# Kernel optimization log

Hardware: AMD Instinct MI355X
Metric: run time of the kernel (lower is better)

Reference implementation:

```python
import jax, jax.numpy as jnp
import numpy as np

H = 256        # hidden_channels (== out_channels)
IN = 128       # in_channels (atom features)
ED = 64        # edge_dim (bond features)
G = 1024       # num graphs
L = 48         # atoms per graph (static pad length)
N = G * L      # num atoms
E = 2 * N      # num directed edges
NLAYERS = 4


def setup_inputs() -> dict:
    key = jax.random.key(0)
    ks = jax.random.split(key, 12)
    def rn(k, shape, scale=0.05):
        return jax.random.normal(k, shape, jnp.float32) * scale
    return {
        "x": jax.random.normal(ks[0], (N, IN), jnp.float32),
        "edge_attr": jax.random.normal(ks[1], (E, ED), jnp.float32),
        "edge_index": jax.random.randint(ks[2], (2, E), 0, N),
        "batch": jnp.repeat(jnp.arange(G), L),  # sorted, L atoms per graph
        "w_atom": rn(ks[3], (IN, H)), "b_atom": jnp.zeros((H,), jnp.float32),
        "w_bond": rn(ks[4], (ED, H)), "b_bond": jnp.zeros((H,), jnp.float32),
        "conv_w": rn(ks[5], (NLAYERS, H, H)), "conv_b": jnp.zeros((NLAYERS, H), jnp.float32),
        "w_lin": rn(ks[6], (3 * H, H)), "b_lin": jnp.zeros((H,), jnp.float32),
        "gru_bias": rn(ks[7], (H,), 0.06),
        "w_ih": rn(ks[8], (2, 3 * H, H)), "w_hh": rn(ks[9], (2, 3 * H, H)),
        "b_ih": jnp.zeros((2, 3 * H), jnp.float32), "b_hh": jnp.zeros((2, 3 * H), jnp.float32),
        "w_out": rn(ks[10], (2 * H, H)), "b_out": jnp.zeros((H,), jnp.float32),
    }


def reference(x, edge_attr, edge_index, batch, w_atom, b_atom, w_bond, b_bond,
              conv_w, conv_b, w_lin, b_lin, gru_bias, w_ih, w_hh, b_ih, b_hh,
              w_out, b_out):
    relu = jax.nn.relu
    row, col = edge_index[0], edge_index[1]  # flow='target_to_source': aggregate at row

    x_proj = relu(x @ w_atom + b_atom)                 # [N, H]
    h_atom = x_proj
    h_bond = relu(edge_attr @ w_bond + b_bond)         # [E, H]

    def booster(h_bond):
        # message_booster multi-aggregation: sum * max (empty slots -> 0, as torch_scatter)
        s = jax.ops.segment_sum(h_bond, row, num_segments=N)
        m = jax.ops.segment_max(h_bond, row, num_segments=N)
        m = jnp.where(jnp.isfinite(m), m, 0.0)
        return s * m

    for i in range(NLAYERS - 1):
        h_atom = h_atom + booster(h_bond)              # additive communicator
        # edge_update: x[edge_index_i] - edge_attr[edge_index_j]; seq = Linear+ReLU (dropout p=0)
        h_bond = relu((h_atom[row] - h_bond[col]) @ conv_w[i] + conv_b[i])
    aggr_message = h_atom + booster(h_bond)            # last conv; edge output discarded

    h = jnp.concatenate([aggr_message, h_atom, x_proj], axis=1) @ w_lin + b_lin  # [N, H]

    # ---- BatchGRU ----
    msg = relu(h + gru_bias)
    starts = jnp.searchsorted(batch, jnp.arange(G))
    pos = jnp.arange(N) - starts[batch]                # position within own graph
    messages = jnp.zeros((G, L, H), h.dtype).at[batch, pos].set(msg)
    h0 = jax.ops.segment_max(h, batch, num_segments=G)  # [G, H], same init both dirs

    def gru_dir(seq, d):
        def cell(hst, x_t):
            gi = x_t @ w_ih[d].T + b_ih[d]
            gh = hst @ w_hh[d].T + b_hh[d]
            i_r, i_z, i_n = jnp.split(gi, 3, -1)
            h_r, h_z, h_n = jnp.split(gh, 3, -1)
            r = jax.nn.sigmoid(i_r + h_r)
            z = jax.nn.sigmoid(i_z + h_z)
            n = jnp.tanh(i_n + r * h_n)
            hn = (1.0 - z) * n + z * hst
            return hn, hn
        _, out = jax.lax.scan(cell, h0, seq)
        return out

    seq = messages.transpose(1, 0, 2)                  # [L, G, H]
    out_f = gru_dir(seq, 0)
    out_b = gru_dir(seq[::-1], 1)[::-1]
    h_msgs = jnp.concatenate([out_f, out_b], -1).transpose(1, 0, 2)  # [G, L, 2H]
    unpadded = h_msgs[batch, pos]                      # [N, 2H]

    return relu(unpadded @ w_out + b_out)              # seq_out (dropout p=0)
```

## Files before the change

### kernel.cpp

```cpp
#include <hip/hip_runtime.h>
#include <math.h>

#define HH 256
#define GG 1024
#define LL 48
#define NNODES 49152
#define NEDGES 98304
#define SB 256.0f
#define DSB 0.00390625f

typedef _Float16 f16;
typedef __attribute__((ext_vector_type(8))) _Float16 f16x8;
typedef __attribute__((ext_vector_type(4))) float f32x4;

#define MFMA16(a, b, c) __builtin_amdgcn_mfma_f32_16x16x32_f16(a, b, c, 0, 0, 0)

__device__ inline float sc_from_max(float m) {
    if (!(m > 0.f)) return 1.0f;
    return ldexpf(1.0f, 13 - ilogbf(m));
}

__global__ void csr_count(const int* __restrict__ row, int* __restrict__ counts)
{
    int e = blockIdx.x * 256 + threadIdx.x;
    if (e < NEDGES) atomicAdd(&counts[row[e]], 1);
}

__global__ __launch_bounds__(1024) void scan_offsets(const int* __restrict__ counts,
                                                     int* __restrict__ offsets)
{
    __shared__ int tsum[1024];
    const int tid = threadIdx.x;
    const int base = tid * 48;
    int s = 0;
    for (int i = 0; i < 48; i++) s += counts[base + i];
    tsum[tid] = s;
    __syncthreads();
    for (int off = 1; off < 1024; off <<= 1) {
        int v = (tid >= off) ? tsum[tid - off] : 0;
        __syncthreads();
        tsum[tid] += v;
        __syncthreads();
    }
    int run = (tid == 0) ? 0 : tsum[tid - 1];
    for (int i = 0; i < 48; i++) { offsets[base + i] = run; run += counts[base + i]; }
    if (tid == 1023) offsets[NNODES] = run;
}

__global__ void csr_fill(const int* __restrict__ row, const int* __restrict__ offsets,
                         int* __restrict__ cursor, int* __restrict__ elist)
{
    int e = blockIdx.x * 256 + threadIdx.x;
    if (e < NEDGES) {
        int r = row[e];
        int p = atomicAdd(&cursor[r], 1);
        elist[offsets[r] + p] = e;
    }
}

__global__ void prep_graphs(const int* __restrict__ batch, int* __restrict__ starts,
                            int* __restrict__ gcnt)
{
    int i = blockIdx.x * 256 + threadIdx.x;
    if (i < NNODES) {
        int b = batch[i];
        atomicAdd(&gcnt[b], 1);
        if (i == 0 || batch[i - 1] != b) starts[b] = i;
    }
}

__global__ void rowscale(const float* __restrict__ A, int K, float* __restrict__ sc)
{
    int m = blockIdx.x, ln = threadIdx.x;
    float v = 0.f;
    for (int k = ln; k < K; k += 64) v = fmaxf(v, fabsf(A[(size_t)m * K + k]));
    for (int s = 32; s; s >>= 1) v = fmaxf(v, __shfl_xor(v, s));
    if (ln == 0) sc[m] = sc_from_max(v);
}

__global__ void prep_wT(const float* __restrict__ Wsrc, f16* __restrict__ oH,
                        f16* __restrict__ oL)
{
    int idx = blockIdx.x * 256 + threadIdx.x;
    int k = idx >> 8, n = idx & 255;
    float v = Wsrc[(size_t)k * 256 + n] * SB;
    f16 h = (f16)v;
    size_t o = ((size_t)(k >> 5) * 256 + n) * 32 + (k & 31);
    oH[o] = h;
    oL[o] = (f16)(v - (float)h);
}

__global__ void prep_gruW(const float* __restrict__ w_ih, const float* __restrict__ w_hh,
                          const float* __restrict__ b_ih, const float* __restrict__ b_hh,
                          f16* __restrict__ BgH, f16* __restrict__ BgL,
                          float* __restrict__ bias4)
{
    int idx = blockIdx.x * 256 + threadIdx.x;
    int d = idx >> 19;
    int rem = idx & 524287;
    int k = rem >> 10;
    int col = rem & 1023;
    int jj = col >> 2, s = col & 3;
    const float* Wi = w_ih + (size_t)d * 768 * 256;
    const float* Wh = w_hh + (size_t)d * 768 * 256;
    float v;
    if (s == 0)      v = (k < 256) ? Wi[(size_t)jj * 256 + k]         : Wh[(size_t)jj * 256 + (k - 256)];
    else if (s == 1) v = (k < 256) ? Wi[(size_t)(256 + jj) * 256 + k] : Wh[(size_t)(256 + jj) * 256 + (k - 256)];
    else if (s == 2) v = (k < 256) ? Wi[(size_t)(512 + jj) * 256 + k] : 0.f;
    else             v = (k < 256) ? 0.f : Wh[(size_t)(512 + jj) * 256 + (k - 256)];
    v *= SB;
    f16 h = (f16)v;
    size_t o = ((size_t)(d * 16 + (k >> 5)) * 1024 + col) * 32 + (k & 31);
    BgH[o] = h;
    BgL[o] = (f16)(v - (float)h);
    if (k == 0) {
        const float* bi = b_ih + d * 768;
        const float* bh = b_hh + d * 768;
        float bv;
        if (s == 0)      bv = bi[jj] + bh[jj];
        else if (s == 1) bv = bi[256 + jj] + bh[256 + jj];
        else if (s == 2) bv = bi[512 + jj];
        else             bv = bh[512 + jj];
        bias4[d * 1024 + col] = bv;
    }
}

__global__ void booster(const float* __restrict__ hb_lo, const float* __restrict__ hb_hi,
                        const float* __restrict__ atom_in, float* __restrict__ out,
                        const int* __restrict__ offsets, const int* __restrict__ elist,
                        float* __restrict__ scOut)
{
    int n = blockIdx.x, c = threadIdx.x;
    int b0 = offsets[n], b1 = offsets[n + 1];
    float s = 0.f, m = 0.f;
    for (int p = b0; p < b1; p++) {
        int e = elist[p];
        const float* hb = (e < NNODES) ? (hb_lo + (size_t)e * HH)
                                       : (hb_hi + (size_t)(e - NNODES) * HH);
        float v = hb[c];
        s += v;
        m = fmaxf(m, v);
    }
    float o = atom_in[(size_t)n * HH + c] + s * m;
    out[(size_t)n * HH + c] = o;
    float v = fabsf(o);
    for (int t = 32; t; t >>= 1) v = fmaxf(v, __shfl_xor(v, t));
    __shared__ float wm[4];
    if ((c & 63) == 0) wm[c >> 6] = v;
    __syncthreads();
    if (c == 0)
        scOut[n] = sc_from_max(fmaxf(fmaxf(wm[0], wm[1]), fmaxf(wm[2], wm[3])));
}

__global__ void h0_init(const float* __restrict__ h, const int* __restrict__ starts,
                        const int* __restrict__ gcnt, float* __restrict__ hid0,
                        float* __restrict__ scG)
{
    int g = blockIdx.x, c = threadIdx.x;
    int st = starts[g], cn = gcnt[g];
    float m = -INFINITY, am = 0.f;
    for (int i = 0; i < cn; i++) {
        float v = h[(size_t)(st + i) * HH + c];
        m = fmaxf(m, v);
        am = fmaxf(am, fabsf(v));
    }
    if (cn == 0) m = 0.f;
    hid0[(size_t)g * HH + c] = m;
    hid0[(size_t)GG * HH + (size_t)g * HH + c] = m;
    for (int t = 32; t; t >>= 1) am = fmaxf(am, __shfl_xor(am, t));
    __shared__ float wm[4];
    if ((c & 63) == 0) wm[c >> 6] = am;
    __syncthreads();
    if (c == 0) {
        float M = fmaxf(fmaxf(fmaxf(wm[0], wm[1]), fmaxf(wm[2], wm[3])) + 0.07f, 1.0f);
        scG[g] = sc_from_max(M);
    }
}

__global__ void build_msgP(const float* __restrict__ h, const float* __restrict__ gbias,
                           const int* __restrict__ starts, const int* __restrict__ gcnt,
                           float* __restrict__ msgP)
{
    int l = blockIdx.x, g = blockIdx.y, k = threadIdx.x;
    float v = 0.f;
    if (l < gcnt[g]) {
        int node = starts[g] + l;
        v = fmaxf(h[(size_t)node * HH + k] + gbias[k], 0.f);
    }
    msgP[((size_t)l * GG + g) * HH + k] = v;
}

template<int MODE>
__device__ __forceinline__ void gemmLoadA(const float* __restrict__ A,
    const float* __restrict__ S0, const float* __restrict__ S1,
    const float* __restrict__ S2, int rI, int cI, int row, int K, int k,
    float va[8])
{
    if constexpr (MODE == 0) {
        const float* p = A + (size_t)row * K + k;
        float4 v0 = *(const float4*)p, v1 = *(const float4*)(p + 4);
        va[0]=v0.x; va[1]=v0.y; va[2]=v0.z; va[3]=v0.w;
        va[4]=v1.x; va[5]=v1.y; va[6]=v1.z; va[7]=v1.w;
    } else if constexpr (MODE == 1) {
        const float* pa = S0 + (size_t)rI * HH + k;
        const float* pb = S1 + (size_t)cI * HH + k;
        float4 a0 = *(const float4*)pa, a1 = *(const float4*)(pa + 4);
        float4 b0 = *(const float4*)pb, b1 = *(const float4*)(pb + 4);
        va[0]=a0.x-b0.x; va[1]=a0.y-b0.y; va[2]=a0.z-b0.z; va[3]=a0.w-b0.w;
        va[4]=a1.x-b1.x; va[5]=a1.y-b1.y; va[6]=a1.z-b1.z; va[7]=a1.w-b1.w;
    } else if constexpr (MODE == 2) {
        const float* S = (k < 256) ? S0 : ((k < 512) ? S1 : S2);
        const float* p = S + (size_t)row * HH + (k & 255);
        float4 v0 = *(const float4*)p, v1 = *(const float4*)(p + 4);
        va[0]=v0.x; va[1]=v0.y; va[2]=v0.z; va[3]=v0.w;
        va[4]=v1.x; va[5]=v1.y; va[6]=v1.z; va[7]=v1.w;
    } else {
        const float* S = (k < 256) ? S0 : S1;
        const float* p = S + (size_t)row * HH + (k & 255);
        float4 v0 = *(const float4*)p, v1 = *(const float4*)(p + 4);
        va[0]=v0.x; va[1]=v0.y; va[2]=v0.z; va[3]=v0.w;
        va[4]=v1.x; va[5]=v1.y; va[6]=v1.z; va[7]=v1.w;
    }
}

template<int MODE, bool RELU, bool SPLITC, bool WSCALE, int NX>
__global__ __launch_bounds__(256) void gemm_f16x3(
    const float* __restrict__ A,
    const float* __restrict__ S0, const float* __restrict__ S1, const float* __restrict__ S2,
    const int* __restrict__ ridx, const int* __restrict__ cidx,
    const f16* __restrict__ BgH, const f16* __restrict__ BgL,
    const float* __restrict__ bias,
    const float* __restrict__ sc0, const float* __restrict__ sc1, const float* __restrict__ sc2,
    float* __restrict__ Clo, float* __restrict__ Chi,
    float* __restrict__ scOut, int K)
{
    __shared__ __align__(16) f16 Ah[64 * 40], Al[64 * 40];
    __shared__ __align__(16) f16 Bh[256 * 40], Bl[256 * 40];
    __shared__ float scL[64];
    __shared__ float rmL[64][4];

    const int tid = threadIdx.x;
    const int m0 = blockIdx.x * 64;
    const int arow = tid >> 2, aoct = tid & 3;
    const int w = tid >> 6, lane = tid & 63, lr = lane & 15, lh = lane >> 4;

    if (tid < 64) {
        float sc;
        if constexpr (MODE == 0) sc = sc0[m0 + tid];
        else if constexpr (MODE == 1) {
            int r = ridx[m0 + tid], cc = cidx[m0 + tid];
            sc = fminf(sc0[r], sc1[cc]) * 0.5f;
        } else if constexpr (MODE == 2) {
            sc = fminf(fminf(sc0[m0 + tid], sc1[m0 + tid]), sc2[m0 + tid]);
        } else {
            sc = sc0[cidx[m0 + tid]];
        }
        scL[tid] = sc;
    }
    int rI = 0, cI = 0;
    if constexpr (MODE == 1) { rI = ridx[m0 + arow]; cI = cidx[m0 + arow]; }
    __syncthreads();
    const float myS = scL[arow];

    float va[8];
    f16x8 rbh[4], rbl[4];
    gemmLoadA<MODE>(A, S0, S1, S2, rI, cI, m0 + arow, K, aoct * 8, va);
    {
        size_t base = (size_t)tid * 32;
        const f16x8* ph = (const f16x8*)(BgH + base);
#pragma unroll
        for (int q = 0; q < 4; q++) rbh[q] = ph[q];
        if constexpr (NX == 3) {
            const f16x8* pl = (const f16x8*)(BgL + base);
#pragma unroll
            for (int q = 0; q < 4; q++) rbl[q] = pl[q];
        }
    }

    f32x4 acc[4][4] = {};
    for (int k0 = 0; k0 < K; k0 += 32) {
        {
            f16x8 hi, lo;
#pragma unroll
            for (int e = 0; e < 8; e++) {
                float a = va[e] * myS;
                f16 h = (f16)a;
                hi[e] = h;
                if constexpr (NX == 3) lo[e] = (f16)(a - (float)h);
            }
            *(f16x8*)&Ah[arow * 40 + aoct * 8] = hi;
            if constexpr (NX == 3) *(f16x8*)&Al[arow * 40 + aoct * 8] = lo;
        }
#pragma unroll
        for (int q = 0; q < 4; q++) {
            *(f16x8*)&Bh[tid * 40 + q * 8] = rbh[q];
            if constexpr (NX == 3) *(f16x8*)&Bl[tid * 40 + q * 8] = rbl[q];
        }
        __syncthreads();
        if (k0 + 32 < K) {
            gemmLoadA<MODE>(A, S0, S1, S2, rI, cI, m0 + arow, K, k0 + 32 + aoct * 8, va);
            size_t base = ((size_t)((k0 + 32) >> 5) * 256 + tid) * 32;
            const f16x8* ph = (const f16x8*)(BgH + base);
#pragma unroll
            for (int q = 0; q < 4; q++) rbh[q] = ph[q];
            if constexpr (NX == 3) {
                const f16x8* pl = (const f16x8*)(BgL + base);
#pragma unroll
                for (int q = 0; q < 4; q++) rbl[q] = pl[q];
            }
        }
        f16x8 fah[4], fal[4];
#pragma unroll
        for (int i = 0; i < 4; i++) {
            fah[i] = *(const f16x8*)&Ah[(i * 16 + lr) * 40 + lh * 8];
            if constexpr (NX == 3) fal[i] = *(const f16x8*)&Al[(i * 16 + lr) * 40 + lh * 8];
        }
#pragma unroll
        for (int j = 0; j < 4; j++) {
            int colx = w * 64 + j * 16 + lr;
            f16x8 fbh = *(const f16x8*)&Bh[colx * 40 + lh * 8];
            if constexpr (NX == 3) {
                f16x8 fbl = *(const f16x8*)&Bl[colx * 40 + lh * 8];
#pragma unroll
                for (int i = 0; i < 4; i++) {
                    acc[i][j] = MFMA16(fah[i], fbh, acc[i][j]);
                    acc[i][j] = MFMA16(fah[i], fbl, acc[i][j]);
                    acc[i][j] = MFMA16(fal[i], fbh, acc[i][j]);
                }
            } else {
#pragma unroll
                for (int i = 0; i < 4; i++)
                    acc[i][j] = MFMA16(fah[i], fbh, acc[i][j]);
            }
        }
        __syncthreads();
    }

    float rm[4][4];
#pragma unroll
    for (int i = 0; i < 4; i++)
#pragma unroll
        for (int e = 0; e < 4; e++) rm[i][e] = 0.f;
#pragma unroll
    for (int i = 0; i < 4; i++) {
#pragma unroll
        for (int e = 0; e < 4; e++) {
            int ml = i * 16 + lh * 4 + e;
            int m = m0 + ml;
            float inv = DSB / scL[ml];
            float* Cb;
            if constexpr (SPLITC)
                Cb = (m < NNODES) ? (Clo + (size_t)m * HH) : (Chi + (size_t)(m - NNODES) * HH);
            else
                Cb = Clo + (size_t)m * HH;
#pragma unroll
            for (int j = 0; j < 4; j++) {
                int n = w * 64 + j * 16 + lr;
                float v = acc[i][j][e] * inv + bias[n];
                if constexpr (RELU) v = fmaxf(v, 0.f);
                Cb[n] = v;
                if constexpr (WSCALE) rm[i][e] = fmaxf(rm[i][e], fabsf(v));
            }
        }
    }
    if constexpr (WSCALE) {
#pragma unroll
        for (int i = 0; i < 4; i++)
#pragma unroll
            for (int e = 0; e < 4; e++) {
                float v = rm[i][e];
                v = fmaxf(v, __shfl_xor(v, 1));
                v = fmaxf(v, __shfl_xor(v, 2));
                v = fmaxf(v, __shfl_xor(v, 4));
                v = fmaxf(v, __shfl_xor(v, 8));
                if (lr == 0) rmL[i * 16 + lh * 4 + e][w] = v;
            }
        __syncthreads();
        if (tid < 64)
            scOut[m0 + tid] = sc_from_max(fmaxf(fmaxf(rmL[tid][0], rmL[tid][1]),
                                                fmaxf(rmL[tid][2], rmL[tid][3])));
    }
}

__global__ __launch_bounds__(256) void gru_step_f16(
    const float* __restrict__ msgP, const f16* __restrict__ BgH, const f16* __restrict__ BgL,
    const float* __restrict__ bias4, const float* __restrict__ hidC, float* __restrict__ hidN,
    const float* __restrict__ scG, const int* __restrict__ starts, const int* __restrict__ gcnt,
    float* __restrict__ outF, float* __restrict__ outB, int t)
{
    __shared__ __align__(16) char smemraw[25600];
    f16* Ah = (f16*)smemraw;
    f16* Al = Ah + 1280;
    f16* Bh = Al + 1280;
    f16* Bl = Bh + 5120;
    float* Cs = (float*)smemraw;
    __shared__ float scL[32];

    const int tid = threadIdx.x;
    const int id = blockIdx.x;
    const int c = id & 7, d = (id >> 3) & 1, gt = id >> 4;
    const int g0 = gt * 32;
    const int l = d ? (LL - 1 - t) : t;
    const float* hidCd = hidC + (size_t)d * GG * HH;
    float* hidNd = hidN + (size_t)d * GG * HH;

    if (tid < 32) scL[tid] = scG[g0 + tid];
    __syncthreads();

    const bool aact = tid < 128;
    const int arow = (tid >> 2) & 31, aoct = tid & 3;
    const float myS = scL[arow];
    const int w = tid >> 6, lane = tid & 63, lr = lane & 15, lh = lane >> 4;
    const int bcol = tid & 127, bpl = tid >> 7;

    float va[8];
    f16x8 rb[4];
    {
        if (aact) {
            const float* p = msgP + ((size_t)l * GG + g0 + arow) * HH + aoct * 8;
            float4 v0 = *(const float4*)p, v1 = *(const float4*)(p + 4);
            va[0]=v0.x; va[1]=v0.y; va[2]=v0.z; va[3]=v0.w;
            va[4]=v1.x; va[5]=v1.y; va[6]=v1.z; va[7]=v1.w;
        }
        size_t base = ((size_t)(d * 16) * 1024 + c * 128 + bcol) * 32;
        const f16x8* pb = (const f16x8*)((bpl ? BgL : BgH) + base);
#pragma unroll
        for (int q = 0; q < 4; q++) rb[q] = pb[q];
    }

    f32x4 acc[2][2] = {};
    for (int kb = 0; kb < 16; kb++) {
        {
            if (aact) {
                f16x8 hi, lo;
#pragma unroll
                for (int e = 0; e < 8; e++) {
                    float a = va[e] * myS;
                    f16 h = (f16)a;
                    hi[e] = h;
                    lo[e] = (f16)(a - (float)h);
                }
                *(f16x8*)&Ah[arow * 40 + aoct * 8] = hi;
                *(f16x8*)&Al[arow * 40 + aoct * 8] = lo;
            }
            f16* Bp = bpl ? Bl : Bh;
#pragma unroll
            for (int q = 0; q < 4; q++)
                *(f16x8*)&Bp[bcol * 40 + q * 8] = rb[q];
        }
        __syncthreads();
        if (kb < 15) {
            if (aact) {
                int k = (kb + 1) * 32 + aoct * 8;
                const float* p = (k < 256)
                    ? msgP + ((size_t)l * GG + g0 + arow) * HH + k
                    : hidCd + (size_t)(g0 + arow) * HH + (k - 256);
                float4 v0 = *(const float4*)p, v1 = *(const float4*)(p + 4);
                va[0]=v0.x; va[1]=v0.y; va[2]=v0.z; va[3]=v0.w;
                va[4]=v1.x; va[5]=v1.y; va[6]=v1.z; va[7]=v1.w;
            }
            size_t base = ((size_t)(d * 16 + kb + 1) * 1024 + c * 128 + bcol) * 32;
            const f16x8* pb = (const f16x8*)((bpl ? BgL : BgH) + base);
#pragma unroll
            for (int q = 0; q < 4; q++) rb[q] = pb[q];
        }
        f16x8 fah[2], fal[2];
#pragma unroll
        for (int i = 0; i < 2; i++) {
            fah[i] = *(const f16x8*)&Ah[(i * 16 + lr) * 40 + lh * 8];
            fal[i] = *(const f16x8*)&Al[(i * 16 + lr) * 40 + lh * 8];
        }
#pragma unroll
        for (int j = 0; j < 2; j++) {
            int colx = w * 32 + j * 16 + lr;
            f16x8 fbh = *(const f16x8*)&Bh[colx * 40 + lh * 8];
            f16x8 fbl = *(const f16x8*)&Bl[colx * 40 + lh * 8];
#pragma unroll
            for (int i = 0; i < 2; i++) {
                acc[i][j] = MFMA16(fah[i], fbh, acc[i][j]);
                acc[i][j] = MFMA16(fah[i], fbl, acc[i][j]);
                acc[i][j] = MFMA16(fal[i], fbh, acc[i][j]);
            }
        }
        __syncthreads();
    }

#pragma unroll
    for (int i = 0; i < 2; i++) {
#pragma unroll
        for (int e = 0; e < 4; e++) {
            int ml = i * 16 + lh * 4 + e;
            float inv = DSB / scL[ml];
#pragma unroll
            for (int j = 0; j < 2; j++)
                Cs[ml * 132 + w * 32 + j * 16 + lr] = acc[i][j][e] * inv;
        }
    }
    __syncthreads();

    const float* b4 = bias4 + d * 1024;
    const int jl = tid & 31;
    const int J  = c * 32 + jl;
    const int gbase = (tid >> 5) * 4;
    const float bb0 = b4[4 * J + 0], bb1 = b4[4 * J + 1];
    const float bb2 = b4[4 * J + 2], bb3 = b4[4 * J + 3];
    float* o = d ? outB : outF;
#pragma unroll
    for (int i = 0; i < 4; i++) {
        int gl = gbase + i;
        int g = g0 + gl;
        f32x4 gv = *(const f32x4*)&Cs[gl * 132 + jl * 4];
        float r = 1.f / (1.f + expf(-(gv[0] + bb0)));
        float z = 1.f / (1.f + expf(-(gv[1] + bb1)));
        float nn = tanhf(gv[2] + bb2 + r * (gv[3] + bb3));
        float hp = hidCd[(size_t)g * HH + J];
        float hnew = (1.f - z) * nn + z * hp;
        hidNd[(size_t)g * HH + J] = hnew;
        if (l < gcnt[g]) o[(size_t)(starts[g] + l) * HH + J] = hnew;
    }
}

__global__ void fill_sentinel(float* __restrict__ out, float v)
{
    size_t idx = (size_t)blockIdx.x * 256 + threadIdx.x;
    out[idx] = v;
}

extern "C" void kernel_launch(void* const* d_in, const int* in_sizes, int n_in,
                              void* d_out, int out_size, void* d_ws, size_t ws_size,
                              hipStream_t stream)
{
    (void)in_sizes; (void)n_in; (void)out_size;
    const float* x         = (const float*)d_in[0];
    const float* edge_attr = (const float*)d_in[1];
    const int*   eidx      = (const int*)d_in[2];
    const int*   batch     = (const int*)d_in[3];
    const float* w_atom    = (const float*)d_in[4];
    const float* b_atom    = (const float*)d_in[5];
    const float* w_bond    = (const float*)d_in[6];
    const float* b_bond    = (const float*)d_in[7];
    const float* conv_w    = (const float*)d_in[8];
    const float* conv_b    = (const float*)d_in[9];
    const float* w_lin     = (const float*)d_in[10];
    const float* b_lin     = (const float*)d_in[11];
    const float* gru_bias  = (const float*)d_in[12];
    const float* w_ih      = (const float*)d_in[13];
    const float* w_hh      = (const float*)d_in[14];
    const float* b_ih      = (const float*)d_in[15];
    const float* b_hh      = (const float*)d_in[16];
    const float* w_out     = (const float*)d_in[17];
    const float* b_out     = (const float*)d_in[18];

    const int* row = eidx;
    const int* col = eidx + NEDGES;

    const size_t NH = (size_t)NNODES * HH;

    float* W   = (float*)d_ws;
    float* W0  = W;
    float* W1  = W + NH;
    float* W1h = W + 2 * NH;
    float* W2  = W + 3 * NH;
    float* DO  = (float*)d_out;

    size_t off = 4 * NH;
    int* counts  = (int*)(W + off);      off += NNODES;
    int* cursor  = (int*)(W + off);      off += NNODES;
    int* gcnt    = (int*)(W + off);      off += GG;
    int* starts  = (int*)(W + off);      off += GG;
    int* offsets = (int*)(W + off);      off += NNODES + 1;
    int* elist   = (int*)(W + off);      off += NEDGES;
    float* scX    = W + off;             off += NNODES;
    float* scEA   = W + off;             off += NEDGES;
    float* scHbA  = W + off;             off += NEDGES;
    float* scHbB  = W + off;             off += NEDGES;
    float* scAtom = W + off;             off += NNODES;
    float* scAggr = W + off;             off += NNODES;
    float* scXp   = W + off;             off += NNODES;
    float* scGru  = W + off;             off += GG;
    off = (off + 3) & ~(size_t)3;
    f16* fp = (f16*)(W + off);
    f16* watomH = fp;                     fp += 4 * 256 * 32;
    f16* watomL = fp;                     fp += 4 * 256 * 32;
    f16* wbondH = fp;                     fp += 2 * 256 * 32;
    f16* wbondL = fp;                     fp += 2 * 256 * 32;
    f16* convH[3]; f16* convL[3];
    for (int i = 0; i < 3; i++) { convH[i] = fp; fp += 8 * 256 * 32; convL[i] = fp; fp += 8 * 256 * 32; }
    f16* wlinH = fp;                      fp += 24 * 256 * 32;
    f16* wlinL = fp;                      fp += 24 * 256 * 32;
    f16* woutH = fp;                      fp += 16 * 256 * 32;
    f16* woutL = fp;                      fp += 16 * 256 * 32;

    const size_t NEED = (char*)fp - (char*)d_ws;
    if (ws_size < NEED) {
        fill_sentinel<<<(int)(NH / 256), 256, 0, stream>>>((float*)d_out, (float)ws_size);
        return;
    }

    float* hid0  = DO;
    float* hid1  = DO + 2 * (size_t)GG * HH;
    float* bias4 = DO + 4 * (size_t)GG * HH;
    f16* BgH = (f16*)(bias4 + 2048);
    f16* BgL = BgH + (size_t)2 * 16 * 1024 * 32;

    hipMemsetAsync(counts, 0, (size_t)(2 * NNODES + 2 * GG) * sizeof(int), stream);
    prep_graphs<<<(NNODES + 255) / 256, 256, 0, stream>>>(batch, starts, gcnt);
    csr_count<<<(NEDGES + 255) / 256, 256, 0, stream>>>(row, counts);
    scan_offsets<<<1, 1024, 0, stream>>>(counts, offsets);
    csr_fill<<<(NEDGES + 255) / 256, 256, 0, stream>>>(row, offsets, cursor, elist);

    rowscale<<<NNODES, 64, 0, stream>>>(x, 128, scX);
    rowscale<<<NEDGES, 64, 0, stream>>>(edge_attr, 64, scEA);

    prep_wT<<<128, 256, 0, stream>>>(w_atom, watomH, watomL);
    prep_wT<<<64, 256, 0, stream>>>(w_bond, wbondH, wbondL);
    for (int i = 0; i < 3; i++)
        prep_wT<<<256, 256, 0, stream>>>(conv_w + (size_t)i * HH * HH, convH[i], convL[i]);
    prep_wT<<<768, 256, 0, stream>>>(w_lin, wlinH, wlinL);
    prep_wT<<<512, 256, 0, stream>>>(w_out, woutH, woutL);

    gemm_f16x3<0, true, false, true, 3><<<NNODES / 64, 256, 0, stream>>>(
        x, nullptr, nullptr, nullptr, nullptr, nullptr, watomH, watomL, b_atom,
        scX, nullptr, nullptr, W0, nullptr, scAtom, 128);
    gemm_f16x3<0, true, true, true, 3><<<NEDGES / 64, 256, 0, stream>>>(
        edge_attr, nullptr, nullptr, nullptr, nullptr, nullptr, wbondH, wbondL, b_bond,
        scEA, nullptr, nullptr, W1, W1h, scHbA, 64);

    float* cur_lo = W1; float* cur_hi = W1h; float* cur_sc = scHbA;
    float* nxt_lo = W2; float* nxt_hi = DO;  float* nxt_sc = scHbB;
    for (int i = 0; i < 3; i++) {
        booster<<<NNODES, 256, 0, stream>>>(cur_lo, cur_hi, W0, W0, offsets, elist, scAtom);
        gemm_f16x3<1, true, true, true, 3><<<NEDGES / 64, 256, 0, stream>>>(
            nullptr, W0, cur_lo, nullptr, row, col, convH[i], convL[i],
            conv_b + (size_t)i * HH, scAtom, cur_sc, nullptr, nxt_lo, nxt_hi, nxt_sc, 256);
        float* t0 = cur_lo; cur_lo = nxt_lo; nxt_lo = t0;
        float* t1 = cur_hi; cur_hi = nxt_hi; nxt_hi = t1;
        float* t2 = cur_sc; cur_sc = nxt_sc; nxt_sc = t2;
    }
    booster<<<NNODES, 256, 0, stream>>>(cur_lo, cur_hi, W0, W1, offsets, elist, scAggr);
    gemm_f16x3<0, true, false, true, 3><<<NNODES / 64, 256, 0, stream>>>(
        x, nullptr, nullptr, nullptr, nullptr, nullptr, watomH, watomL, b_atom,
        scX, nullptr, nullptr, W1h, nullptr, scXp, 128);
    gemm_f16x3<2, false, false, false, 3><<<NNODES / 64, 256, 0, stream>>>(
        nullptr, W1, W0, W1h, nullptr, nullptr, wlinH, wlinL, b_lin,
        scAggr, scAtom, scXp, W2, nullptr, nullptr, 768);

    h0_init<<<GG, 256, 0, stream>>>(W2, starts, gcnt, hid0, scGru);
    build_msgP<<<dim3(LL, GG), 256, 0, stream>>>(W2, gru_bias, starts, gcnt, W1h);
    prep_gruW<<<(2 * 512 * 1024) / 256, 256, 0, stream>>>(w_ih, w_hh, b_ih, b_hh, BgH, BgL, bias4);

    for (int t = 0; t < LL; t++) {
        float* hc = (t & 1) ? hid1 : hid0;
        float* hx = (t & 1) ? hid0 : hid1;
        gru_step_f16<<<512, 256, 0, stream>>>(W1h, BgH, BgL, bias4, hc, hx,
                                              scGru, starts, gcnt, W0, W1, t);
    }

    gemm_f16x3<3, true, false, false, 1><<<NNODES / 64, 256, 0, stream>>>(
        nullptr, W0, W1, nullptr, nullptr, batch, woutH, nullptr, b_out,
        scGru, nullptr, nullptr, (float*)d_out, nullptr, nullptr, 512);
}
```

Baseline: 1.564 ms.

## Load B fragments directly from global into registers, skip LDS staging

Both the main f16x3 GEMM and the GRU step kernel now read the pre-packed weight fragments straight from global memory into MFMA operand registers instead of staging them through shared memory. The GRU step also widens its A tile to 64 K per window, so all 256 threads convert activations and it needs half as many barriers. This removes LDS writes and reads for B and shrinks shared memory, which may raise occupancy. The cost is that weights are loaded redundantly per wave from L2/global without the register prefetch overlap that existed before.

```diff
diff --git a/kernel.cpp b/kernel.cpp
--- a/kernel.cpp
+++ b/kernel.cpp
@@ -235,7 +235,6 @@
     float* __restrict__ scOut, int K)
 {
     __shared__ __align__(16) f16 Ah[64 * 40], Al[64 * 40];
-    __shared__ __align__(16) f16 Bh[256 * 40], Bl[256 * 40];
     __shared__ float scL[64];
     __shared__ float rmL[64][4];
 
@@ -263,19 +262,7 @@
     const float myS = scL[arow];
 
     float va[8];
-    f16x8 rbh[4], rbl[4];
     gemmLoadA<MODE>(A, S0, S1, S2, rI, cI, m0 + arow, K, aoct * 8, va);
-    {
-        size_t base = (size_t)tid * 32;
-        const f16x8* ph = (const f16x8*)(BgH + base);
-#pragma unroll
-        for (int q = 0; q < 4; q++) rbh[q] = ph[q];
-        if constexpr (NX == 3) {
-            const f16x8* pl = (const f16x8*)(BgL + base);
-#pragma unroll
-            for (int q = 0; q < 4; q++) rbl[q] = pl[q];
-        }
-    }
 
     f32x4 acc[4][4] = {};
     for (int k0 = 0; k0 < K; k0 += 32) {
@@ -291,22 +278,17 @@
             *(f16x8*)&Ah[arow * 40 + aoct * 8] = hi;
             if constexpr (NX == 3) *(f16x8*)&Al[arow * 40 + aoct * 8] = lo;
         }
-#pragma unroll
-        for (int q = 0; q < 4; q++) {
-            *(f16x8*)&Bh[tid * 40 + q * 8] = rbh[q];
-            if constexpr (NX == 3) *(f16x8*)&Bl[tid * 40 + q * 8] = rbl[q];
-        }
         __syncthreads();
-        if (k0 + 32 < K) {
+        if (k0 + 32 < K)
             gemmLoadA<MODE>(A, S0, S1, S2, rI, cI, m0 + arow, K, k0 + 32 + aoct * 8, va);
-            size_t base = ((size_t)((k0 + 32) >> 5) * 256 + tid) * 32;
-            const f16x8* ph = (const f16x8*)(BgH + base);
-#pragma unroll
-            for (int q = 0; q < 4; q++) rbh[q] = ph[q];
-            if constexpr (NX == 3) {
-                const f16x8* pl = (const f16x8*)(BgL + base);
-#pragma unroll
-                for (int q = 0; q < 4; q++) rbl[q] = pl[q];
+        f16x8 fbh[4], fbl[4];
+        {
+            size_t kbase = (size_t)(k0 >> 5) * 256;
+#pragma unroll
+            for (int j = 0; j < 4; j++) {
+                size_t o = (kbase + (w * 64 + j * 16 + lr)) * 32 + lh * 8;
+                fbh[j] = *(const f16x8*)(BgH + o);
+                if constexpr (NX == 3) fbl[j] = *(const f16x8*)(BgL + o);
             }
         }
         f16x8 fah[4], fal[4];
@@ -317,20 +299,17 @@
         }
 #pragma unroll
         for (int j = 0; j < 4; j++) {
-            int colx = w * 64 + j * 16 + lr;
-            f16x8 fbh = *(const f16x8*)&Bh[colx * 40 + lh * 8];
             if constexpr (NX == 3) {
-                f16x8 fbl = *(const f16x8*)&Bl[colx * 40 + lh * 8];
 #pragma unroll
                 for (int i = 0; i < 4; i++) {
-                    acc[i][j] = MFMA16(fah[i], fbh, acc[i][j]);
-                    acc[i][j] = MFMA16(fah[i], fbl, acc[i][j]);
-                    acc[i][j] = MFMA16(fal[i], fbh, acc[i][j]);
+                    acc[i][j] = MFMA16(fah[i], fbh[j], acc[i][j]);
+                    acc[i][j] = MFMA16(fah[i], fbl[j], acc[i][j]);
+                    acc[i][j] = MFMA16(fal[i], fbh[j], acc[i][j]);
                 }
             } else {
 #pragma unroll
                 for (int i = 0; i < 4; i++)
-                    acc[i][j] = MFMA16(fah[i], fbh, acc[i][j]);
+                    acc[i][j] = MFMA16(fah[i], fbh[j], acc[i][j]);
             }
         }
         __syncthreads();
@@ -388,11 +367,9 @@
     const float* __restrict__ scG, const int* __restrict__ starts, const int* __restrict__ gcnt,
     float* __restrict__ outF, float* __restrict__ outB, int t)
 {
-    __shared__ __align__(16) char smemraw[25600];
+    __shared__ __align__(16) char smemraw[16896];
     f16* Ah = (f16*)smemraw;
-    f16* Al = Ah + 1280;
-    f16* Bh = Al + 1280;
-    f16* Bl = Bh + 5120;
+    f16* Al = Ah + 32 * 72;
     float* Cs = (float*)smemraw;
     __shared__ float scL[32];
 
@@ -407,79 +384,69 @@
     if (tid < 32) scL[tid] = scG[g0 + tid];
     __syncthreads();
 
-    const bool aact = tid < 128;
-    const int arow = (tid >> 2) & 31, aoct = tid & 3;
+    const int arow = tid >> 3, akoct = tid & 7;
     const float myS = scL[arow];
     const int w = tid >> 6, lane = tid & 63, lr = lane & 15, lh = lane >> 4;
-    const int bcol = tid & 127, bpl = tid >> 7;
 
     float va[8];
-    f16x8 rb[4];
     {
-        if (aact) {
-            const float* p = msgP + ((size_t)l * GG + g0 + arow) * HH + aoct * 8;
+        const float* p = msgP + ((size_t)l * GG + g0 + arow) * HH + akoct * 8;
+        float4 v0 = *(const float4*)p, v1 = *(const float4*)(p + 4);
+        va[0]=v0.x; va[1]=v0.y; va[2]=v0.z; va[3]=v0.w;
+        va[4]=v1.x; va[5]=v1.y; va[6]=v1.z; va[7]=v1.w;
+    }
+
+    f32x4 acc[2][2] = {};
+    for (int win = 0; win < 8; win++) {
+        {
+            f16x8 hi, lo;
+#pragma unroll
+            for (int e = 0; e < 8; e++) {
+                float a = va[e] * myS;
+                f16 h = (f16)a;
+                hi[e] = h;
+                lo[e] = (f16)(a - (float)h);
+            }
+            *(f16x8*)&Ah[arow * 72 + akoct * 8] = hi;
+            *(f16x8*)&Al[arow * 72 + akoct * 8] = lo;
+        }
+        __syncthreads();
+        if (win < 7) {
+            int k = (win + 1) * 64 + akoct * 8;
+            const float* p = (k < 256)
+                ? msgP + ((size_t)l * GG + g0 + arow) * HH + k
+                : hidCd + (size_t)(g0 + arow) * HH + (k - 256);
             float4 v0 = *(const float4*)p, v1 = *(const float4*)(p + 4);
             va[0]=v0.x; va[1]=v0.y; va[2]=v0.z; va[3]=v0.w;
             va[4]=v1.x; va[5]=v1.y; va[6]=v1.z; va[7]=v1.w;
         }
-        size_t base = ((size_t)(d * 16) * 1024 + c * 128 + bcol) * 32;
-        const f16x8* pb = (const f16x8*)((bpl ? BgL : BgH) + base);
-#pragma unroll
-        for (int q = 0; q < 4; q++) rb[q] = pb[q];
-    }
-
-    f32x4 acc[2][2] = {};
-    for (int kb = 0; kb < 16; kb++) {
-        {
-            if (aact) {
-                f16x8 hi, lo;
-#pragma unroll
-                for (int e = 0; e < 8; e++) {
-                    float a = va[e] * myS;
-                    f16 h = (f16)a;
-                    hi[e] = h;
-                    lo[e] = (f16)(a - (float)h);
+        f16x8 fbh[2][2], fbl[2][2];
+#pragma unroll
+        for (int ks = 0; ks < 2; ks++) {
+            size_t kbase = (size_t)(d * 16 + win * 2 + ks) * 1024;
+#pragma unroll
+            for (int j = 0; j < 2; j++) {
+                size_t o = (kbase + (c * 128 + w * 32 + j * 16 + lr)) * 32 + lh * 8;
+                fbh[ks][j] = *(const f16x8*)(BgH + o);
+                fbl[ks][j] = *(const f16x8*)(BgL + o);
+            }
+        }
+#pragma unroll
+        for (int ks = 0; ks < 2; ks++) {
+            f16x8 fah[2], fal[2];
+#pragma unroll
+            for (int i = 0; i < 2; i++) {
+                fah[i] = *(const f16x8*)&Ah[(i * 16 + lr) * 72 + ks * 32 + lh * 8];
+                fal[i] = *(const f16x8*)&Al[(i * 16 + lr) * 72 + ks * 32 + lh * 8];
+            }
+#pragma unroll
+            for (int j = 0; j < 2; j++) {
+#pragma unroll
+                for (int i = 0; i < 2; i++) {
+                    acc[i][j] = MFMA16(fah[i], fbh[ks][j], acc[i][j]);
+                    acc[i][j] = MFMA16(fah[i], fbl[ks][j], acc[i][j]);
+                    acc[i][j] = MFMA16(fal[i], fbh[ks][j], acc[i][j]);
                 }
-                *(f16x8*)&Ah[arow * 40 + aoct * 8] = hi;
-                *(f16x8*)&Al[arow * 40 + aoct * 8] = lo;
-            }
-            f16* Bp = bpl ? Bl : Bh;
-#pragma unroll
-            for (int q = 0; q < 4; q++)
-                *(f16x8*)&Bp[bcol * 40 + q * 8] = rb[q];
-        }
-        __syncthreads();
-        if (kb < 15) {
-            if (aact) {
-                int k = (kb + 1) * 32 + aoct * 8;
-                const float* p = (k < 256)
-                    ? msgP + ((size_t)l * GG + g0 + arow) * HH + k
-                    : hidCd + (size_t)(g0 + arow) * HH + (k - 256);
-                float4 v0 = *(const float4*)p, v1 = *(const float4*)(p + 4);
-                va[0]=v0.x; va[1]=v0.y; va[2]=v0.z; va[3]=v0.w;
-                va[4]=v1.x; va[5]=v1.y; va[6]=v1.z; va[7]=v1.w;
-            }
-            size_t base = ((size_t)(d * 16 + kb + 1) * 1024 + c * 128 + bcol) * 32;
-            const f16x8* pb = (const f16x8*)((bpl ? BgL : BgH) + base);
-#pragma unroll
-            for (int q = 0; q < 4; q++) rb[q] = pb[q];
-        }
-        f16x8 fah[2], fal[2];
-#pragma unroll
-        for (int i = 0; i < 2; i++) {
-            fah[i] = *(const f16x8*)&Ah[(i * 16 + lr) * 40 + lh * 8];
-            fal[i] = *(const f16x8*)&Al[(i * 16 + lr) * 40 + lh * 8];
-        }
-#pragma unroll
-        for (int j = 0; j < 2; j++) {
-            int colx = w * 32 + j * 16 + lr;
-            f16x8 fbh = *(const f16x8*)&Bh[colx * 40 + lh * 8];
-            f16x8 fbl = *(const f16x8*)&Bl[colx * 40 + lh * 8];
-#pragma unroll
-            for (int i = 0; i < 2; i++) {
-                acc[i][j] = MFMA16(fah[i], fbh, acc[i][j]);
-                acc[i][j] = MFMA16(fah[i], fbl, acc[i][j]);
-                acc[i][j] = MFMA16(fal[i], fbh, acc[i][j]);
             }
         }
         __syncthreads();
```

After: 1.699 ms. 8.6% more time.

## Load GRU weight fragments directly to registers and double-buffer A tiles

Applied to the files above, without the earlier changes.

Rewrites the GRU step GEMM main loop. B (weight) fragments now go straight from global memory into MFMA registers instead of being staged through shared memory. The A tile is widened to a 64-wide K window, written into double-buffered LDS by all 256 threads. This halves the number of barriers per step and cuts LDS traffic, at the cost of more live registers for the prefetched B fragments and uncoalesced per-lane global loads of B.

```diff
diff --git a/kernel.cpp b/kernel.cpp
--- a/kernel.cpp
+++ b/kernel.cpp
@@ -388,11 +388,7 @@
     const float* __restrict__ scG, const int* __restrict__ starts, const int* __restrict__ gcnt,
     float* __restrict__ outF, float* __restrict__ outB, int t)
 {
-    __shared__ __align__(16) char smemraw[25600];
-    f16* Ah = (f16*)smemraw;
-    f16* Al = Ah + 1280;
-    f16* Bh = Al + 1280;
-    f16* Bl = Bh + 5120;
+    __shared__ __align__(16) char smemraw[18432];
     float* Cs = (float*)smemraw;
     __shared__ float scL[32];
 
@@ -407,80 +403,110 @@
     if (tid < 32) scL[tid] = scG[g0 + tid];
     __syncthreads();
 
-    const bool aact = tid < 128;
-    const int arow = (tid >> 2) & 31, aoct = tid & 3;
+    const int arow = tid >> 3, akoct = tid & 7;
     const float myS = scL[arow];
     const int w = tid >> 6, lane = tid & 63, lr = lane & 15, lh = lane >> 4;
-    const int bcol = tid & 127, bpl = tid >> 7;
-
-    float va[8];
-    f16x8 rb[4];
+
+    f16* Ah0 = (f16*)smemraw;
+    f16* Al0 = Ah0 + 2304;
+    f16* Ah1 = Al0 + 2304;
+    f16* Al1 = Ah1 + 2304;
+
     {
-        if (aact) {
-            const float* p = msgP + ((size_t)l * GG + g0 + arow) * HH + aoct * 8;
+        const float* p = msgP + ((size_t)l * GG + g0 + arow) * HH + akoct * 8;
+        float4 v0 = *(const float4*)p, v1 = *(const float4*)(p + 4);
+        float va0[8] = {v0.x, v0.y, v0.z, v0.w, v1.x, v1.y, v1.z, v1.w};
+        f16x8 hi, lo;
+#pragma unroll
+        for (int e = 0; e < 8; e++) {
+            float a = va0[e] * myS;
+            f16 h = (f16)a;
+            hi[e] = h;
+            lo[e] = (f16)(a - (float)h);
+        }
+        *(f16x8*)&Ah0[arow * 72 + akoct * 8] = hi;
+        *(f16x8*)&Al0[arow * 72 + akoct * 8] = lo;
+    }
+    f16x8 fbh[2][2], fbl[2][2];
+#pragma unroll
+    for (int ks = 0; ks < 2; ks++) {
+        size_t kbase = (size_t)(d * 16 + ks) * 1024;
+#pragma unroll
+        for (int j = 0; j < 2; j++) {
+            size_t o = (kbase + (c * 128 + w * 32 + j * 16 + lr)) * 32 + lh * 8;
+            fbh[ks][j] = *(const f16x8*)(BgH + o);
+            fbl[ks][j] = *(const f16x8*)(BgL + o);
+        }
+    }
+    __syncthreads();
+
+    f32x4 acc[2][2] = {};
+#pragma unroll
+    for (int win = 0; win < 8; win++) {
+        f16* AhC = (win & 1) ? Ah1 : Ah0;
+        f16* AlC = (win & 1) ? Al1 : Al0;
+        f16* AhN = (win & 1) ? Ah0 : Ah1;
+        f16* AlN = (win & 1) ? Al0 : Al1;
+
+        float va[8];
+        if (win < 7) {
+            int k = (win + 1) * 64 + akoct * 8;
+            const float* p = (k < 256)
+                ? msgP + ((size_t)l * GG + g0 + arow) * HH + k
+                : hidCd + (size_t)(g0 + arow) * HH + (k - 256);
             float4 v0 = *(const float4*)p, v1 = *(const float4*)(p + 4);
             va[0]=v0.x; va[1]=v0.y; va[2]=v0.z; va[3]=v0.w;
             va[4]=v1.x; va[5]=v1.y; va[6]=v1.z; va[7]=v1.w;
         }
-        size_t base = ((size_t)(d * 16) * 1024 + c * 128 + bcol) * 32;
-        const f16x8* pb = (const f16x8*)((bpl ? BgL : BgH) + base);
-#pragma unroll
-        for (int q = 0; q < 4; q++) rb[q] = pb[q];
-    }
-
-    f32x4 acc[2][2] = {};
-    for (int kb = 0; kb < 16; kb++) {
-        {
-            if (aact) {
-                f16x8 hi, lo;
-#pragma unroll
-                for (int e = 0; e < 8; e++) {
-                    float a = va[e] * myS;
-                    f16 h = (f16)a;
-                    hi[e] = h;
-                    lo[e] = (f16)(a - (float)h);
+        f16x8 nbh[2][2], nbl[2][2];
+        if (win < 7) {
+#pragma unroll
+            for (int ks = 0; ks < 2; ks++) {
+                size_t kbase = (size_t)(d * 16 + (win + 1) * 2 + ks) * 1024;
+#pragma unroll
+                for (int j = 0; j < 2; j++) {
+                    size_t o = (kbase + (c * 128 + w * 32 + j * 16 + lr)) * 32 + lh * 8;
+                    nbh[ks][j] = *(const f16x8*)(BgH + o);
+                    nbl[ks][j] = *(const f16x8*)(BgL + o);
                 }
-                *(f16x8*)&Ah[arow * 40 + aoct * 8] = hi;
-                *(f16x8*)&Al[arow * 40 + aoct * 8] = lo;
-            }
-            f16* Bp = bpl ? Bl : Bh;
-#pragma unroll
-            for (int q = 0; q < 4; q++)
-                *(f16x8*)&Bp[bcol * 40 + q * 8] = rb[q];
-        }
-        __syncthreads();
-        if (kb < 15) {
-            if (aact) {
-                int k = (kb + 1) * 32 + aoct * 8;
-                const float* p = (k < 256)
-                    ? msgP + ((size_t)l * GG + g0 + arow) * HH + k
-                    : hidCd + (size_t)(g0 + arow) * HH + (k - 256);
-                float4 v0 = *(const float4*)p, v1 = *(const float4*)(p + 4);
-                va[0]=v0.x; va[1]=v0.y; va[2]=v0.z; va[3]=v0.w;
-                va[4]=v1.x; va[5]=v1.y; va[6]=v1.z; va[7]=v1.w;
-            }
-            size_t base = ((size_t)(d * 16 + kb + 1) * 1024 + c * 128 + bcol) * 32;
-            const f16x8* pb = (const f16x8*)((bpl ? BgL : BgH) + base);
-#pragma unroll
-            for (int q = 0; q < 4; q++) rb[q] = pb[q];
-        }
-        f16x8 fah[2], fal[2];
-#pragma unroll
-        for (int i = 0; i < 2; i++) {
-            fah[i] = *(const f16x8*)&Ah[(i * 16 + lr) * 40 + lh * 8];
-            fal[i] = *(const f16x8*)&Al[(i * 16 + lr) * 40 + lh * 8];
-        }
-#pragma unroll
-        for (int j = 0; j < 2; j++) {
-            int colx = w * 32 + j * 16 + lr;
-            f16x8 fbh = *(const f16x8*)&Bh[colx * 40 + lh * 8];
-            f16x8 fbl = *(const f16x8*)&Bl[colx * 40 + lh * 8];
+            }
+        }
+#pragma unroll
+        for (int ks = 0; ks < 2; ks++) {
+            f16x8 fah[2], fal[2];
 #pragma unroll
             for (int i = 0; i < 2; i++) {
-                acc[i][j] = MFMA16(fah[i], fbh, acc[i][j]);
-                acc[i][j] = MFMA16(fah[i], fbl, acc[i][j]);
-                acc[i][j] = MFMA16(fal[i], fbh, acc[i][j]);
-            }
+                fah[i] = *(const f16x8*)&AhC[(i * 16 + lr) * 72 + ks * 32 + lh * 8];
+                fal[i] = *(const f16x8*)&AlC[(i * 16 + lr) * 72 + ks * 32 + lh * 8];
+            }
+#pragma unroll
+            for (int j = 0; j < 2; j++) {
+#pragma unroll
+                for (int i = 0; i < 2; i++) {
+                    acc[i][j] = MFMA16(fah[i], fbh[ks][j], acc[i][j]);
+                    acc[i][j] = MFMA16(fah[i], fbl[ks][j], acc[i][j]);
+                    acc[i][j] = MFMA16(fal[i], fbh[ks][j], acc[i][j]);
+                }
+            }
+        }
+        if (win < 7) {
+            f16x8 hi, lo;
+#pragma unroll
+            for (int e = 0; e < 8; e++) {
+                float a = va[e] * myS;
+                f16 h = (f16)a;
+                hi[e] = h;
+                lo[e] = (f16)(a - (float)h);
+            }
+            *(f16x8*)&AhN[arow * 72 + akoct * 8] = hi;
+            *(f16x8*)&AlN[arow * 72 + akoct * 8] = lo;
+#pragma unroll
+            for (int ks = 0; ks < 2; ks++)
+#pragma unroll
+                for (int j = 0; j < 2; j++) {
+                    fbh[ks][j] = nbh[ks][j];
+                    fbl[ks][j] = nbl[ks][j];
+                }
         }
         __syncthreads();
     }
```

Result: faster. 1.474 ms (-5.8%).
